# Performance work log

Measured on AMD Instinct MI355X. Metric: run time of the kernel, lower is better.

## Reference

```python
import jax, jax.numpy as jnp
import numpy as np

B, S, D, H = 4, 2048, 1024, 16
DK = D // H


def setup_inputs() -> dict:
    key = jax.random.key(0)
    ks = jax.random.split(key, 9)
    sc = 1.0 / np.sqrt(D)
    return {
        "query": jax.random.normal(ks[0], (B, S, D), jnp.float32),
        "key": jax.random.normal(ks[1], (B, S, D), jnp.float32),
        "value": jax.random.normal(ks[2], (B, S, D), jnp.float32),
        "Wq": jax.random.normal(ks[3], (D, D), jnp.float32) * sc,
        "bq": jax.random.normal(ks[4], (D,), jnp.float32) * sc,
        "Wk": jax.random.normal(ks[5], (D, D), jnp.float32) * sc,
        "bk": jax.random.normal(ks[6], (D,), jnp.float32) * sc,
        "Wv": jax.random.normal(ks[7], (D, D), jnp.float32) * sc,
        "bv": jax.random.normal(ks[8], (D,), jnp.float32) * sc,
    }


def reference(query, key, value, Wq, bq, Wk, bk, Wv, bv):
    # QKV projections, split into heads: [B,S,D] -> [B,H,S,DK]
    q = (query @ Wq + bq).reshape(B, S, H, DK).transpose(0, 2, 1, 3)
    k = (key @ Wk + bk).reshape(B, S, H, DK).transpose(0, 2, 1, 3)
    v = (value @ Wv + bv).reshape(B, S, H, DK).transpose(0, 2, 1, 3)
    # NOTE: original module applies NO 1/sqrt(d_k) scaling
    attn = jnp.einsum("bhqd,bhkd->bhqk", q, k)
    attn = jax.nn.softmax(attn, axis=-1)  # dropout is identity at inference
    ctx = jnp.einsum("bhqk,bhkd->bhqd", attn, v)
    ctx = ctx.transpose(0, 2, 1, 3).reshape(B, S, D)
    # original adds residual to raw concatenated context (no output projection)
    return ctx + query
```

## Files before the change

### kernel.cpp

```cpp
#include <hip/hip_runtime.h>
#include <hip/hip_bf16.h>
#include <stdint.h>

#define Bb 4
#define Ss 2048
#define Dd 1024
#define Hh 16
#define DK 64
#define BH 64
#define Mm 8192
#define KVT 64

typedef __attribute__((ext_vector_type(8))) _Float16 f16x8;
typedef __attribute__((ext_vector_type(4))) _Float16 f16x4;
typedef __attribute__((ext_vector_type(2))) __fp16 fp16x2;
typedef __attribute__((ext_vector_type(4))) float f32x4;
typedef __attribute__((ext_vector_type(16))) float f32x16;
typedef __attribute__((ext_vector_type(2))) unsigned uint2v;

__device__ __forceinline__ void gload16(const _Float16* g, _Float16* lds) {
  __builtin_amdgcn_global_load_lds((const __attribute__((address_space(1))) unsigned int*)g,
                                   (__attribute__((address_space(3))) unsigned int*)lds, 16, 0, 0);
}

#if __has_builtin(__builtin_amdgcn_exp2f)
__device__ __forceinline__ float ex2(float x) { return __builtin_amdgcn_exp2f(x); }
#else
__device__ __forceinline__ float ex2(float x) {
  float r; asm("v_exp_f32 %0, %1" : "=v"(r) : "v"(x)); return r;
}
#endif

__device__ __forceinline__ unsigned pk2u(float a, float b) {
  union { fp16x2 h; unsigned u; } x;
  x.h = __builtin_amdgcn_cvt_pkrtz(a, b);
  return x.u;
}

__device__ __forceinline__ float xhalf_max(float x) {
  union { float f; unsigned u; } a; a.f = x;
  uint2v r = __builtin_amdgcn_permlane32_swap(a.u, a.u, false, false);
  union { unsigned u; float f; } b0, b1; b0.u = r[0]; b1.u = r[1];
  return fmaxf(fmaxf(x, b0.f), b1.f);
}

__global__ __launch_bounds__(256) void cvt_wt(const float* __restrict__ wq,
                                              const float* __restrict__ wk,
                                              const float* __restrict__ wv,
                                              _Float16* __restrict__ tq,
                                              _Float16* __restrict__ tk,
                                              _Float16* __restrict__ tv) {
  const float* w = blockIdx.z == 0 ? wq : (blockIdx.z == 1 ? wk : wv);
  _Float16* o = blockIdx.z == 0 ? tq : (blockIdx.z == 1 ? tk : tv);
  float wscale = blockIdx.z == 0 ? 1.4426950408889634f : 1.0f;
  __shared__ float tile[64][65];
  int k0 = blockIdx.x * 64;
  int n0 = blockIdx.y * 64;
  int t = threadIdx.x;
  int tr = t >> 4;
  int tc = (t & 15) * 4;
  for (int i = 0; i < 4; i++) {
    int r = i * 16 + tr;
    float4 val = *(const float4*)(w + (k0 + r) * Dd + n0 + tc);
    tile[r][tc + 0] = val.x; tile[r][tc + 1] = val.y;
    tile[r][tc + 2] = val.z; tile[r][tc + 3] = val.w;
  }
  __syncthreads();
  for (int i = 0; i < 2; i++) {
    int vdx = t + 256 * i;
    int rn = vdx >> 3;
    int c8 = (vdx & 7) * 8;
    union { f16x8 v8; _Float16 h[8]; } o2;
    for (int j = 0; j < 8; j++) o2.h[j] = (_Float16)(tile[c8 + j][rn] * wscale);
    *(f16x8*)(o + (n0 + rn) * Dd + k0 + c8) = o2.v8;
  }
}

__global__ __launch_bounds__(256) void gemm_qkv(
    const float* __restrict__ aq, const float* __restrict__ ak,
    const float* __restrict__ av,
    const _Float16* __restrict__ wtq, const _Float16* __restrict__ wtk,
    const _Float16* __restrict__ wtv,
    const float* __restrict__ bq, const float* __restrict__ bk, const float* __restrict__ bv,
    _Float16* __restrict__ oq, _Float16* __restrict__ ok,
    _Float16* __restrict__ ov) {
  int z = blockIdx.z;
  const float* Af    = z == 0 ? aq  : (z == 1 ? ak  : av);
  const _Float16* Bt = z == 0 ? wtq : (z == 1 ? wtk : wtv);
  const float* bias  = z == 0 ? bq  : (z == 1 ? bk  : bv);
  _Float16* out      = z == 0 ? oq  : (z == 1 ? ok  : ov);
  float bscale       = z == 0 ? 1.4426950408889634f : 1.0f;

  __shared__ _Float16 As[128 * 64];
  __shared__ _Float16 Bs[128 * 64];

  int tid = threadIdx.x;
  int w = tid >> 6;
  int l = tid & 63;
  int lr = l & 15, lk = l >> 4;
  int m0 = blockIdx.x * 128;
  int n0 = blockIdx.y * 128;
  int wr = (w >> 1) * 64;
  int wc = (w & 1) * 64;

  f32x4 acc[4][4] = {};

  for (int kt = 0; kt < Dd; kt += 64) {
    __syncthreads();
    for (int i = 0; i < 4; i++) {
      int fbase = i * 256 + w * 64;
      int f = fbase + l;
      int r = f >> 3, c = (f & 7) * 8;
      gload16(Bt + (n0 + r) * Dd + kt + c, &Bs[fbase * 8]);
      const float* ap = Af + (size_t)(m0 + r) * Dd + kt + c;
      float4 a0 = *(const float4*)ap;
      float4 a1 = *(const float4*)(ap + 4);
      union { unsigned u[4]; f16x8 v; } aw;
      aw.u[0] = pk2u(a0.x, a0.y); aw.u[1] = pk2u(a0.z, a0.w);
      aw.u[2] = pk2u(a1.x, a1.y); aw.u[3] = pk2u(a1.z, a1.w);
      *(f16x8*)&As[f * 8] = aw.v;
    }
    __syncthreads();
    for (int kh = 0; kh < 2; kh++) {
      f16x8 af[4], bfr[4];
      for (int mi = 0; mi < 4; mi++)
        af[mi] = *(const f16x8*)&As[(wr + mi * 16 + lr) * 64 + kh * 32 + lk * 8];
      for (int ni = 0; ni < 4; ni++)
        bfr[ni] = *(const f16x8*)&Bs[(wc + ni * 16 + lr) * 64 + kh * 32 + lk * 8];
      for (int mi = 0; mi < 4; mi++)
        for (int ni = 0; ni < 4; ni++)
          acc[mi][ni] = __builtin_amdgcn_mfma_f32_16x16x32_f16(af[mi], bfr[ni], acc[mi][ni], 0, 0, 0);
    }
  }

  if (z == 2) {
    for (int mi = 0; mi < 4; mi++) {
      for (int ni = 0; ni < 4; ni++) {
        int n = n0 + wc + ni * 16 + lr;
        float bval = bias[n];
        int h = n >> 6, dk = n & 63;
        int m = m0 + wr + mi * 16 + lk * 4;
        int b = m >> 11, s = m & 2047;
        f16x4 o4;
        for (int j = 0; j < 4; j++) o4[j] = (_Float16)(acc[mi][ni][j] + bval);
        *(f16x4*)(out + ((size_t)((b * Hh + h) * DK + dk) * Ss + s)) = o4;
      }
    }
  } else {
    for (int mi = 0; mi < 4; mi++) {
      for (int ni = 0; ni < 4; ni++) {
        int n = n0 + wc + ni * 16 + lr;
        float bval = bias[n] * bscale;
        int h = n >> 6, dk = n & 63;
        for (int j = 0; j < 4; j++) {
          int m = m0 + wr + mi * 16 + lk * 4 + j;
          int b = m >> 11, s = m & 2047;
          out[((b * Hh + h) * Ss + s) * DK + dk] = (_Float16)(acc[mi][ni][j] + bval);
        }
      }
    }
  }
}

__global__ __launch_bounds__(256) void attn(const _Float16* __restrict__ Qb,
                                            const _Float16* __restrict__ Kb,
                                            const _Float16* __restrict__ Vt,
                                            const float* __restrict__ query,
                                            float* __restrict__ outp) {
  __shared__ _Float16 Kl[2][KVT * 64];
  __shared__ _Float16 Vl[2][KVT * 64];

  int tid = threadIdx.x;
  int w = tid >> 6, l = tid & 63;
  int l31 = l & 31, hi = l >> 5;
  int bh = blockIdx.x;
  int q0 = blockIdx.y * 128 + w * 32;
  const _Float16* Qp = Qb + bh * (Ss * DK);
  const _Float16* Kp = Kb + bh * (Ss * DK);
  const _Float16* Vp = Vt + bh * (DK * Ss);

  int srow = l >> 3;
  int sslot = (l & 7) ^ (srow & 7);
  int w16 = w * 16;
  const _Float16* kp0 = Kp + (w16 + srow) * DK + sslot * 8;
  const _Float16* kp1 = Kp + (w16 + 8 + srow) * DK + sslot * 8;
  const _Float16* vp0 = Vp + (w16 + srow) * Ss + sslot * 8;
  const _Float16* vp1 = Vp + (w16 + 8 + srow) * Ss + sslot * 8;

#define STAGE(BUF)                                                        \
  {                                                                       \
    gload16(kp0, &Kl[BUF][w16 * 64]);                                     \
    gload16(kp1, &Kl[BUF][(w16 + 8) * 64]);                               \
    gload16(vp0, &Vl[BUF][w16 * 64]);                                     \
    gload16(vp1, &Vl[BUF][(w16 + 8) * 64]);                               \
    kp0 += KVT * DK; kp1 += KVT * DK; vp0 += KVT; vp1 += KVT;             \
  }

  f16x8 qf[4];
#pragma unroll
  for (int s = 0; s < 4; s++)
    qf[s] = *(const f16x8*)(Qp + (q0 + l31) * DK + s * 16 + hi * 8);

  f32x16 o0 = {}, o1 = {};
  float mrun = -1e30f, lrun = 0.f;

  int kv7 = l31 & 7;
  int rslot[4];
#pragma unroll
  for (int s = 0; s < 4; s++) rslot[s] = ((s * 2 + hi) ^ kv7) * 8;

#define TILE(BUF)                                                               \
  {                                                                             \
    f32x16 s0 = {}, s1 = {};                                                    \
    _Pragma("unroll")                                                           \
    for (int s = 0; s < 4; s++) {                                               \
      f16x8 ka = *(const f16x8*)&Kl[BUF][l31 * 64 + rslot[s]];                  \
      s0 = __builtin_amdgcn_mfma_f32_32x32x16_f16(ka, qf[s], s0, 0, 0, 0);      \
    }                                                                           \
    _Pragma("unroll")                                                           \
    for (int s = 0; s < 4; s++) {                                               \
      f16x8 kb = *(const f16x8*)&Kl[BUF][(32 + l31) * 64 + rslot[s]];           \
      s1 = __builtin_amdgcn_mfma_f32_32x32x16_f16(kb, qf[s], s1, 0, 0, 0);      \
    }                                                                           \
    float m8[8];                                                                \
    _Pragma("unroll")                                                           \
    for (int r = 0; r < 8; r++)                                                 \
      m8[r] = fmaxf(fmaxf(s0[r], s0[r + 8]), fmaxf(s1[r], s1[r + 8]));          \
    _Pragma("unroll")                                                           \
    for (int d = 4; d >= 1; d >>= 1)                                            \
      for (int r = 0; r < 4; r++) if (r < d) m8[r] = fmaxf(m8[r], m8[r + d]);   \
    float pm = xhalf_max(m8[0]);                                                \
    if (!__all(pm - mrun <= 8.f)) {            \
      float mn = fmaxf(mrun, pm);                                               \
      float sc_ = ex2(mrun - mn);                                               \
      mrun = mn;                                                                \
      lrun *= sc_;                                                              \
      _Pragma("unroll")                                                         \
      for (int r = 0; r < 16; r++) { o0[r] *= sc_; o1[r] *= sc_; }              \
    }                                                                           \
    _Pragma("unroll")                                                           \
    for (int r = 0; r < 16; r++) {                                              \
      s0[r] = ex2(s0[r] - mrun);                                                \
      s1[r] = ex2(s1[r] - mrun);                                                \
    }                                                                           \
    float s8[8];                                                                \
    _Pragma("unroll")                                                           \
    for (int r = 0; r < 8; r++) s8[r] = (s0[r] + s0[r + 8]) + (s1[r] + s1[r + 8]); \
    _Pragma("unroll")                                                           \
    for (int d = 4; d >= 1; d >>= 1)                                            \
      for (int r = 0; r < 4; r++) if (r < d) s8[r] += s8[r + d];                \
    lrun += s8[0];                                                              \
    PVSTEP(BUF, s0, 0, 0)                                                       \
    PVSTEP(BUF, s0, 8, 1)                                                       \
    PVSTEP(BUF, s1, 0, 2)                                                       \
    PVSTEP(BUF, s1, 8, 3)                                                       \
  }

#define PVSTEP(BUF, SRC, OFF, KST)                                              \
    {                                                                           \
      unsigned a0 = pk2u(SRC[(OFF) + 0], SRC[(OFF) + 1]);                       \
      unsigned a1 = pk2u(SRC[(OFF) + 2], SRC[(OFF) + 3]);                       \
      unsigned b0 = pk2u(SRC[(OFF) + 4], SRC[(OFF) + 5]);                       \
      unsigned b1 = pk2u(SRC[(OFF) + 6], SRC[(OFF) + 7]);                       \
      uint2v r0 = __builtin_amdgcn_permlane32_swap(a0, b0, false, false);       \
      uint2v r1 = __builtin_amdgcn_permlane32_swap(a1, b1, false, false);       \
      union { unsigned u[4]; f16x8 v; } pf;                                     \
      pf.u[0] = r0[0]; pf.u[1] = r1[0]; pf.u[2] = r0[1]; pf.u[3] = r1[1];       \
      f16x8 v0 = *(const f16x8*)&Vl[BUF][l31 * 64 + rslot[KST]];                \
      f16x8 v1 = *(const f16x8*)&Vl[BUF][(32 + l31) * 64 + rslot[KST]];         \
      o0 = __builtin_amdgcn_mfma_f32_32x32x16_f16(v0, pf.v, o0, 0, 0, 0);       \
      o1 = __builtin_amdgcn_mfma_f32_32x32x16_f16(v1, pf.v, o1, 0, 0, 0);       \
    }

  STAGE(0)
  __syncthreads();

  for (int it = 0; it < 15; ++it) {
    STAGE(1)
    TILE(0)
    __syncthreads();
    STAGE(0)
    TILE(1)
    __syncthreads();
  }
  STAGE(1)
  TILE(0)
  __syncthreads();
  TILE(1)
#undef PVSTEP
#undef TILE
#undef STAGE

  lrun += __shfl_xor(lrun, 32);
  int b = bh >> 4, h = bh & 15;
  float inv = 1.f / lrun;
  int base = (b * Ss + q0 + l31) * Dd + h * 64;
#pragma unroll
  for (int rq = 0; rq < 4; rq++) {
    int d0 = rq * 8 + hi * 4;
    float4 qv0 = *(const float4*)(query + base + d0);
    float4 ov0;
    ov0.x = o0[rq * 4 + 0] * inv + qv0.x;
    ov0.y = o0[rq * 4 + 1] * inv + qv0.y;
    ov0.z = o0[rq * 4 + 2] * inv + qv0.z;
    ov0.w = o0[rq * 4 + 3] * inv + qv0.w;
    *(float4*)(outp + base + d0) = ov0;
    float4 qv1 = *(const float4*)(query + base + 32 + d0);
    float4 ov1;
    ov1.x = o1[rq * 4 + 0] * inv + qv1.x;
    ov1.y = o1[rq * 4 + 1] * inv + qv1.y;
    ov1.z = o1[rq * 4 + 2] * inv + qv1.z;
    ov1.w = o1[rq * 4 + 3] * inv + qv1.w;
    *(float4*)(outp + base + 32 + d0) = ov1;
  }
}

extern "C" void kernel_launch(void* const* d_in, const int* in_sizes, int n_in,
                              void* d_out, int out_size, void* d_ws, size_t ws_size,
                              hipStream_t stream) {
  const float* query = (const float*)d_in[0];
  const float* key   = (const float*)d_in[1];
  const float* value = (const float*)d_in[2];
  const float* Wq = (const float*)d_in[3];
  const float* bq = (const float*)d_in[4];
  const float* Wk = (const float*)d_in[5];
  const float* bk = (const float*)d_in[6];
  const float* Wv = (const float*)d_in[7];
  const float* bv = (const float*)d_in[8];
  float* out = (float*)d_out;

  _Float16* ws = (_Float16*)d_ws;
  const size_t ACT = (size_t)Mm * Dd;
  const size_t WSZ = (size_t)Dd * Dd;
  _Float16* Wtq  = ws;
  _Float16* Wtk  = Wtq + WSZ;
  _Float16* Wtv  = Wtk + WSZ;
  _Float16* Qb   = Wtv + WSZ;
  _Float16* Kb   = Qb + ACT;
  _Float16* VtT  = Kb + ACT;

  cvt_wt<<<dim3(16, 16, 3), dim3(256), 0, stream>>>(Wq, Wk, Wv, Wtq, Wtk, Wtv);
  gemm_qkv<<<dim3(64, 8, 3), dim3(256), 0, stream>>>(query, key, value, Wtq, Wtk, Wtv,
                                                     bq, bk, bv, Qb, Kb, VtT);
  attn<<<dim3(64, 16), dim3(256), 0, stream>>>(Qb, Kb, VtT, query, out);
}
```

Measured before the change: 203.2 us.

## Double-buffer QKV GEMM LDS tiles with XOR-swizzled layout

Restructures the QKV projection GEMM main loop into a two-stage software pipeline. The next K tile's fp32 A loads and B DMA-to-LDS are issued before the MFMA compute on the current buffer, with one barrier per tile instead of two. It also XOR-swizzles the 16-byte column chunks in LDS to reduce bank conflicts on the fragment reads. The cost is double the LDS footprint (64KB per block), which may lower occupancy, plus more live registers for the prefetched A data.

```diff
diff --git a/kernel.cpp b/kernel.cpp
--- a/kernel.cpp
+++ b/kernel.cpp
@@ -91,8 +91,8 @@
   _Float16* out      = z == 0 ? oq  : (z == 1 ? ok  : ov);
   float bscale       = z == 0 ? 1.4426950408889634f : 1.0f;
 
-  __shared__ _Float16 As[128 * 64];
-  __shared__ _Float16 Bs[128 * 64];
+  __shared__ _Float16 As[2][128 * 64];
+  __shared__ _Float16 Bs[2][128 * 64];
 
   int tid = threadIdx.x;
   int w = tid >> 6;
@@ -103,35 +103,102 @@
   int wr = (w >> 1) * 64;
   int wc = (w & 1) * 64;
 
+  int srow = l >> 3;
+  int cs = (l & 7) ^ srow;
+  const float*    ap[4];
+  const _Float16* bp[4];
+#pragma unroll
+  for (int i = 0; i < 4; i++) {
+    int row = i * 32 + w * 8 + srow;
+    ap[i] = Af + (size_t)(m0 + row) * Dd + cs * 8;
+    bp[i] = Bt + (size_t)(n0 + row) * Dd + cs * 8;
+  }
+
   f32x4 acc[4][4] = {};
-
-  for (int kt = 0; kt < Dd; kt += 64) {
-    __syncthreads();
-    for (int i = 0; i < 4; i++) {
-      int fbase = i * 256 + w * 64;
-      int f = fbase + l;
-      int r = f >> 3, c = (f & 7) * 8;
-      gload16(Bt + (n0 + r) * Dd + kt + c, &Bs[fbase * 8]);
-      const float* ap = Af + (size_t)(m0 + r) * Dd + kt + c;
-      float4 a0 = *(const float4*)ap;
-      float4 a1 = *(const float4*)(ap + 4);
-      union { unsigned u[4]; f16x8 v; } aw;
-      aw.u[0] = pk2u(a0.x, a0.y); aw.u[1] = pk2u(a0.z, a0.w);
-      aw.u[2] = pk2u(a1.x, a1.y); aw.u[3] = pk2u(a1.z, a1.w);
-      *(f16x8*)&As[f * 8] = aw.v;
+  int lr7 = lr & 7;
+  int rs0 = (lk ^ lr7) * 8;
+  int rs1 = ((4 + lk) ^ lr7) * 8;
+
+#define ALOAD(AR)                                                         \
+  _Pragma("unroll")                                                       \
+  for (int i = 0; i < 4; i++) {                                           \
+    AR[i][0] = *(const float4*)(ap[i]);                                   \
+    AR[i][1] = *(const float4*)(ap[i] + 4);                               \
+    ap[i] += 64;                                                          \
+  }
+#define BDMA(NXT)                                                         \
+  _Pragma("unroll")                                                       \
+  for (int i = 0; i < 4; i++) {                                           \
+    gload16(bp[i], &Bs[NXT][(i * 256 + w * 64) * 8]);                     \
+    bp[i] += 64;                                                          \
+  }
+#define AWRITE(AR, NXT)                                                   \
+  _Pragma("unroll")                                                       \
+  for (int i = 0; i < 4; i++) {                                           \
+    union { unsigned u[4]; f16x8 v; } aw;                                 \
+    aw.u[0] = pk2u(AR[i][0].x, AR[i][0].y);                               \
+    aw.u[1] = pk2u(AR[i][0].z, AR[i][0].w);                               \
+    aw.u[2] = pk2u(AR[i][1].x, AR[i][1].y);                               \
+    aw.u[3] = pk2u(AR[i][1].z, AR[i][1].w);                               \
+    *(f16x8*)&As[NXT][(i * 256 + w * 64 + l) * 8] = aw.v;                 \
+  }
+#define GCOMP(CUR)                                                              \
+  _Pragma("unroll")                                                             \
+  for (int kh = 0; kh < 2; kh++) {                                              \
+    int rs = kh ? rs1 : rs0;                                                    \
+    f16x8 af[4], bf[4];                                                         \
+    _Pragma("unroll")                                                           \
+    for (int mi = 0; mi < 4; mi++)                                              \
+      af[mi] = *(const f16x8*)&As[CUR][(wr + mi * 16 + lr) * 64 + rs];          \
+    _Pragma("unroll")                                                           \
+    for (int ni = 0; ni < 4; ni++)                                              \
+      bf[ni] = *(const f16x8*)&Bs[CUR][(wc + ni * 16 + lr) * 64 + rs];          \
+    _Pragma("unroll")                                                           \
+    for (int mi = 0; mi < 4; mi++)                                              \
+      _Pragma("unroll")                                                         \
+      for (int ni = 0; ni < 4; ni++)                                            \
+        acc[mi][ni] = __builtin_amdgcn_mfma_f32_16x16x32_f16(af[mi], bf[ni], acc[mi][ni], 0, 0, 0); \
+  }
+
+  {
+    float4 ar[4][2];
+    ALOAD(ar)
+    BDMA(0)
+    AWRITE(ar, 0)
+  }
+  __syncthreads();
+
+  for (int it = 0; it < 7; ++it) {
+    {
+      float4 ar[4][2];
+      ALOAD(ar)
+      BDMA(1)
+      GCOMP(0)
+      AWRITE(ar, 1)
     }
     __syncthreads();
-    for (int kh = 0; kh < 2; kh++) {
-      f16x8 af[4], bfr[4];
-      for (int mi = 0; mi < 4; mi++)
-        af[mi] = *(const f16x8*)&As[(wr + mi * 16 + lr) * 64 + kh * 32 + lk * 8];
-      for (int ni = 0; ni < 4; ni++)
-        bfr[ni] = *(const f16x8*)&Bs[(wc + ni * 16 + lr) * 64 + kh * 32 + lk * 8];
-      for (int mi = 0; mi < 4; mi++)
-        for (int ni = 0; ni < 4; ni++)
-          acc[mi][ni] = __builtin_amdgcn_mfma_f32_16x16x32_f16(af[mi], bfr[ni], acc[mi][ni], 0, 0, 0);
+    {
+      float4 ar[4][2];
+      ALOAD(ar)
+      BDMA(0)
+      GCOMP(1)
+      AWRITE(ar, 0)
     }
-  }
+    __syncthreads();
+  }
+  {
+    float4 ar[4][2];
+    ALOAD(ar)
+    BDMA(1)
+    GCOMP(0)
+    AWRITE(ar, 1)
+  }
+  __syncthreads();
+  GCOMP(1)
+#undef GCOMP
+#undef AWRITE
+#undef BDMA
+#undef ALOAD
 
   if (z == 2) {
     for (int mi = 0; mi < 4; mi++) {
```

Result: faster. 195.4 us, median of 2 (-3.9%).
